# Kernel tuning notes

Measured on AMD Instinct MI355X. Metric: run time of the kernel, lower is better.

The kernel has to match this reference:

```python
import jax, jax.numpy as jnp
import numpy as np

CLIP = 100000.0
T, N, C, H, E = 8, 1024, 64, 256, 32768
NC = N * (N + 1) // 2


def _ntn(t):
    return jnp.nan_to_num(t, nan=0.0, posinf=CLIP, neginf=-CLIP)


def _gcn_conv(x, row, col, ew, W, b, n):
    # PyG GCNConv: sym-normalized aggregation (self-loops already appended)
    h = x @ W  # [n, out]
    deg = jax.ops.segment_sum(ew, col, num_segments=n)
    dinv = jnp.where(deg > 0, jax.lax.rsqrt(jnp.where(deg > 0, deg, 1.0)), 0.0)
    norm = dinv[row] * ew * dinv[col]  # [e]
    out = jax.ops.segment_sum(norm[:, None] * h[row], col, num_segments=n)
    return out + b


def setup_inputs() -> dict:
    key = jax.random.key(0)
    ks = jax.random.split(key, 10)
    return {
        "xs": jax.random.normal(ks[0], (T, N, C), jnp.float32),
        "edge_index": jax.random.randint(ks[1], (T, 2, E), 0, N),
        "edge_weight": jax.random.uniform(ks[2], (T, E), jnp.float32),
        "conv1_w": jax.random.normal(ks[3], (C, H), jnp.float32) * 0.05,
        "conv1_b": jnp.zeros((H,), jnp.float32),
        "conv2_w": jax.random.normal(ks[4], (H, H), jnp.float32) * 0.05,
        "conv2_b": jnp.zeros((H,), jnp.float32),
        "w_ih": jax.random.normal(ks[5], (4 * H, H), jnp.float32) * 0.05,
        "w_hh": jax.random.normal(ks[6], (4 * H, H), jnp.float32) * 0.05,
        "b_ih": jnp.zeros((4 * H,), jnp.float32),
        "b_hh": jnp.zeros((4 * H,), jnp.float32),
        "fc_w": jax.random.normal(ks[7], (H, NC), jnp.float32) * 0.02,
        "fc_b": jnp.zeros((NC,), jnp.float32),
    }


def reference(xs, edge_index, edge_weight, conv1_w, conv1_b, conv2_w, conv2_b,
              w_ih, w_hh, b_ih, b_hh, fc_w, fc_b):
    n = xs.shape[1]
    self_idx = jnp.arange(n)

    def per_step(x, ei, ew):
        # add self-loops with weight 1 (GCNConv default)
        row = jnp.concatenate([ei[0], self_idx])
        col = jnp.concatenate([ei[1], self_idx])
        w = jnp.concatenate([ew, jnp.ones((n,), ew.dtype)])
        h = jax.nn.relu(_ntn(_gcn_conv(x, row, col, w, conv1_w, conv1_b, n)))
        h = jax.nn.relu(_ntn(_gcn_conv(h, row, col, w, conv2_w, conv2_b, n)))
        return _ntn(h.mean(axis=0))  # global mean pool, single graph

    embs = _ntn(jax.vmap(per_step)(xs, edge_index, edge_weight))  # [T, H]

    def lstm_step(carry, x_t):
        h, c = carry
        g = x_t @ w_ih.T + b_ih + h @ w_hh.T + b_hh
        i, f, gg, o = jnp.split(g, 4)
        c = jax.nn.sigmoid(f) * c + jax.nn.sigmoid(i) * jnp.tanh(gg)
        h = jax.nn.sigmoid(o) * jnp.tanh(c)
        return (h, c), h

    hdim = w_hh.shape[1]
    init = (jnp.zeros((hdim,), embs.dtype), jnp.zeros((hdim,), embs.dtype))
    _, hs = jax.lax.scan(lstm_step, init, embs)
    final_h = _ntn(_ntn(hs)[-1])  # [H]

    vec = _ntn(final_h @ fc_w + fc_b)  # [N(N+1)/2]
    tril = jnp.tril_indices(n)  # row-major (i, j<=i) matches torch loop
    L = jnp.zeros((n, n), vec.dtype).at[tril].set(vec)
    return _ntn(L @ L.T)
```

## Files before the change

### kernel.cpp

```cpp
#include <hip/hip_runtime.h>
#include <hip/hip_bf16.h>
#include <math.h>

#define T_ 8
#define N_ 1024
#define C_ 64
#define H_ 256
#define E_ 32768
#define NC_ 524800
#define SLACK 96
#define CLIPV 100000.0f

__device__ __forceinline__ float sigmoidf_(float x) { return 1.0f / (1.0f + __expf(-x)); }

__global__ void scatter_direct_kernel(const int* __restrict__ ei, const float* __restrict__ ew,
                                      float* __restrict__ deg, int* __restrict__ cnt,
                                      int* __restrict__ csr_src, float* __restrict__ csr_ew) {
    int g = blockIdx.x * 256 + threadIdx.x;
    int t = g >> 15, e = g & (E_ - 1);
    int row = ei[t * 2 * E_ + e];
    int col = ei[t * 2 * E_ + E_ + e];
    float w = ew[g];
    int bin = t * N_ + col;
    atomicAdd(&deg[bin], w);
    int pos = atomicAdd(&cnt[bin], 1);
    if (pos < SLACK) {
        csr_src[bin * SLACK + pos] = row;
        csr_ew[bin * SLACK + pos] = w;
    }
}

__global__ __launch_bounds__(256) void sgemm_nn(const float* __restrict__ A,
                                                const float* __restrict__ B,
                                                float* __restrict__ C,
                                                int M, int N, int K) {
    __shared__ float As[16][68];
    __shared__ float Bs[16][68];
    int tid = threadIdx.x;
    int tx = tid & 15, ty = tid >> 4;
    int m0 = blockIdx.y * 64, n0 = blockIdx.x * 64;
    float acc[4][4] = {{0.f}};
    for (int k0 = 0; k0 < K; k0 += 16) {
        int ka = tid & 15, ma = tid >> 4;
#pragma unroll
        for (int mm = 0; mm < 64; mm += 16)
            As[ka][ma + mm] = A[(size_t)(m0 + ma + mm) * K + k0 + ka];
        int nb = tid & 63, kb = tid >> 6;
#pragma unroll
        for (int kk = 0; kk < 16; kk += 4)
            Bs[kb + kk][nb] = B[(size_t)(k0 + kb + kk) * N + n0 + nb];
        __syncthreads();
#pragma unroll
        for (int kk = 0; kk < 16; ++kk) {
            float4 a4 = *(const float4*)&As[kk][ty * 4];
            float4 b4 = *(const float4*)&Bs[kk][tx * 4];
            float a[4] = {a4.x, a4.y, a4.z, a4.w};
            float b[4] = {b4.x, b4.y, b4.z, b4.w};
#pragma unroll
            for (int i = 0; i < 4; ++i)
#pragma unroll
                for (int j = 0; j < 4; ++j) acc[i][j] += a[i] * b[j];
        }
        __syncthreads();
    }
#pragma unroll
    for (int i = 0; i < 4; ++i) {
        float4 o = make_float4(acc[i][0], acc[i][1], acc[i][2], acc[i][3]);
        *(float4*)&C[(size_t)(m0 + ty * 4 + i) * N + n0 + tx * 4] = o;
    }
}

template <bool POOL>
__global__ __launch_bounds__(256) void agg_kernel(const float* __restrict__ hin,
                                                  const float* __restrict__ deg,
                                                  const int* __restrict__ cnt,
                                                  const int* __restrict__ csr_src,
                                                  const float* __restrict__ csr_ew,
                                                  const float* __restrict__ bias,
                                                  float* __restrict__ out) {
    __shared__ int s_src[SLACK];
    __shared__ float s_nrm[SLACK];
    int bx = blockIdx.x;
    int t = bx >> 10, j = bx & 1023;
    int c = threadIdx.x;
    float dj = rsqrtf(deg[bx] + 1.0f);
    int count = min(cnt[bx], SLACK);
    const float* hbase = hin + (size_t)(t * N_) * H_;
    const float* dbase = deg + t * N_;
    float self = hin[(size_t)bx * H_ + c];
    if (c < count) {
        int s = csr_src[bx * SLACK + c];
        s_src[c] = s;
        s_nrm[c] = csr_ew[bx * SLACK + c] * rsqrtf(dbase[s] + 1.0f);
    }
    __syncthreads();
    float a0 = 0.f, a1 = 0.f, a2 = 0.f, a3 = 0.f;
    int u = 0;
    for (; u + 3 < count; u += 4) {
        int s0 = s_src[u], s1 = s_src[u + 1], s2 = s_src[u + 2], s3 = s_src[u + 3];
        float n0 = s_nrm[u], n1 = s_nrm[u + 1], n2 = s_nrm[u + 2], n3 = s_nrm[u + 3];
        a0 += n0 * hbase[(size_t)s0 * H_ + c];
        a1 += n1 * hbase[(size_t)s1 * H_ + c];
        a2 += n2 * hbase[(size_t)s2 * H_ + c];
        a3 += n3 * hbase[(size_t)s3 * H_ + c];
    }
    for (; u < count; ++u) a0 += s_nrm[u] * hbase[(size_t)s_src[u] * H_ + c];
    float accE = (a0 + a1) + (a2 + a3);
    float val = dj * (dj * self + accE) + bias[c];
    val = fminf(fmaxf(val, 0.0f), CLIPV);
    if (POOL)
        atomicAdd(&out[(size_t)(t * 32 + (j & 31)) * H_ + c], val * (1.0f / 1024.0f));
    else
        out[(size_t)bx * H_ + c] = val;
}

__global__ __launch_bounds__(256) void xg_pool_kernel(const float* __restrict__ pool_part,
                                                      const float* __restrict__ w_ih,
                                                      const float* __restrict__ b_ih,
                                                      const float* __restrict__ b_hh,
                                                      float* __restrict__ xg) {
    __shared__ float s_e[H_];
    int b = blockIdx.x;
    int t = b >> 2;
    int tid = threadIdx.x;
    int j = (b & 3) * 256 + tid;
    float a = 0.f;
#pragma unroll
    for (int g2 = 0; g2 < 32; ++g2) a += pool_part[(size_t)(t * 32 + g2) * H_ + tid];
    s_e[tid] = fminf(fmaxf(a, -CLIPV), CLIPV);
    __syncthreads();
    const float4* wr = (const float4*)(w_ih + (size_t)j * H_);
    float acc = b_ih[j] + b_hh[j];
#pragma unroll 4
    for (int k4 = 0; k4 < H_ / 4; ++k4) {
        float4 w = wr[k4];
        acc += w.x * s_e[k4 * 4] + w.y * s_e[k4 * 4 + 1] + w.z * s_e[k4 * 4 + 2] + w.w * s_e[k4 * 4 + 3];
    }
    xg[t * 1024 + j] = acc;
}

__device__ __forceinline__ void gbar(int* bar, int target) {
    __syncthreads();
    if (threadIdx.x == 0) {
        __threadfence();
        __hip_atomic_fetch_add(bar, 1, __ATOMIC_ACQ_REL, __HIP_MEMORY_SCOPE_AGENT);
        long spin = 0;
        while (__hip_atomic_load(bar, __ATOMIC_ACQUIRE, __HIP_MEMORY_SCOPE_AGENT) < target) {
            if (++spin > (1L << 27)) break;
        }
    }
    __syncthreads();
}

__global__ __launch_bounds__(1024) void lstm_all_kernel(const float* __restrict__ xg,
                                                        const float* __restrict__ w_hh,
                                                        float* __restrict__ gbuf,
                                                        int* __restrict__ bar,
                                                        float* __restrict__ final_h) {
    __shared__ float s_h[H_];
    int tid = threadIdx.x;
    int jl = tid >> 2, q = tid & 3;
    int j = blockIdx.x * 256 + jl;
    float4 wreg[16];
    const float4* wr = (const float4*)(w_hh + (size_t)j * H_ + q * 64);
#pragma unroll
    for (int r = 0; r < 16; ++r) wreg[r] = wr[r];
    float c_reg = 0.f;
    for (int s = 0; s < T_; ++s) {
        if (s == 0) {
            if (tid < 256) s_h[tid] = 0.f;
        } else {
            if (tid < 256) {
                const float* gp = gbuf + ((s - 1) & 1) * 1024;
                float gi = gp[tid], gf = gp[256 + tid], gg = gp[512 + tid], go = gp[768 + tid];
                c_reg = sigmoidf_(gf) * c_reg + sigmoidf_(gi) * tanhf(gg);
                s_h[tid] = sigmoidf_(go) * tanhf(c_reg);
            }
        }
        __syncthreads();
        float acc = 0.f;
#pragma unroll
        for (int r = 0; r < 16; ++r) {
            float4 w = wreg[r];
            int k = q * 64 + r * 4;
            acc += w.x * s_h[k] + w.y * s_h[k + 1] + w.z * s_h[k + 2] + w.w * s_h[k + 3];
        }
        acc += __shfl_xor(acc, 1);
        acc += __shfl_xor(acc, 2);
        if (q == 0) gbuf[(s & 1) * 1024 + j] = xg[s * 1024 + j] + acc;
        gbar(bar, 4 * (s + 1));
    }
    if (blockIdx.x == 0 && tid < 256) {
        const float* gp = gbuf + ((T_ - 1) & 1) * 1024;
        float gi = gp[tid], gf = gp[256 + tid], gg = gp[512 + tid], go = gp[768 + tid];
        float cc = sigmoidf_(gf) * c_reg + sigmoidf_(gi) * tanhf(gg);
        final_h[tid] = sigmoidf_(go) * tanhf(cc);
    }
}

__device__ __forceinline__ void store_quad(float4 v, int j0, float* __restrict__ Lm) {
    int i = (int)((sqrtf(8.0f * (float)j0 + 1.0f) - 1.0f) * 0.5f);
    while ((i + 1) * (i + 2) / 2 <= j0) ++i;
    while (i * (i + 1) / 2 > j0) --i;
    int rb = i * (i + 1) / 2, col = j0 - rb;
    if (col + 3 <= i) {
        *(float4*)&Lm[(size_t)i * 1024 + col] = v;
    } else {
        float vv[4] = {v.x, v.y, v.z, v.w};
#pragma unroll
        for (int e = 0; e < 4; ++e) {
            int jj = j0 + e;
            while ((i + 1) * (i + 2) / 2 <= jj) ++i;
            Lm[(size_t)i * 1024 + (jj - i * (i + 1) / 2)] = vv[e];
        }
    }
}

__global__ __launch_bounds__(256) void fc_kernel(const float* __restrict__ final_h,
                                                 const float* __restrict__ fc_w,
                                                 const float* __restrict__ fc_b,
                                                 float* __restrict__ Lm) {
    __shared__ float s_h[H_];
    __shared__ float4 s_red[256];
    int tid = threadIdx.x;
    s_h[tid] = final_h[tid];
    __syncthreads();
    const int NQ = NC_ / 4;
    int lane = tid & 63, grp = tid >> 6;
    int j4 = blockIdx.x * 64 + lane;
    const float4* w4 = (const float4*)fc_w;
    float4 acc = make_float4(0.f, 0.f, 0.f, 0.f);
    int k0 = grp * 64;
#pragma unroll 8
    for (int i = 0; i < 64; ++i) {
        int k = k0 + i;
        float4 w = w4[(size_t)k * NQ + j4];
        float hk = s_h[k];
        acc.x += hk * w.x; acc.y += hk * w.y; acc.z += hk * w.z; acc.w += hk * w.w;
    }
    s_red[tid] = acc;
    __syncthreads();
    if (tid < 64) {
        float4 a0 = s_red[tid], a1 = s_red[64 + tid], a2 = s_red[128 + tid], a3 = s_red[192 + tid];
        float4 b = ((const float4*)fc_b)[j4];
        float4 r;
        r.x = a0.x + a1.x + a2.x + a3.x + b.x;
        r.y = a0.y + a1.y + a2.y + a3.y + b.y;
        r.z = a0.z + a1.z + a2.z + a3.z + b.z;
        r.w = a0.w + a1.w + a2.w + a3.w + b.w;
        r.x = fminf(fmaxf(r.x, -CLIPV), CLIPV);
        r.y = fminf(fmaxf(r.y, -CLIPV), CLIPV);
        r.z = fminf(fmaxf(r.z, -CLIPV), CLIPV);
        r.w = fminf(fmaxf(r.w, -CLIPV), CLIPV);
        store_quad(r, j4 * 4, Lm);
    }
}

__global__ __launch_bounds__(256) void syrk_kernel(const float* __restrict__ L, float* __restrict__ Cout) {
    int b = blockIdx.x;
    int I = (int)((sqrtf(8.0f * b + 1.0f) - 1.0f) * 0.5f);
    while ((I + 1) * (I + 2) / 2 <= b) ++I;
    while (I * (I + 1) / 2 > b) --I;
    int J = b - I * (I + 1) / 2;
    int Klim = (J + 1) * 64;
    int kbeg = blockIdx.y * 256;
    int kend = min(Klim, kbeg + 256);
    if (kbeg >= kend) return;

    __shared__ float As[16][68];
    __shared__ float Bs[16][68];
    int tid = threadIdx.x;
    int tx = tid & 15, ty = tid >> 4;
    int m0 = I * 64, n0 = J * 64;
    float acc[4][4] = {{0.f}};
    for (int k0 = kbeg; k0 < kend; k0 += 16) {
        int ka = tid & 15, ma = tid >> 4;
#pragma unroll
        for (int mm = 0; mm < 64; mm += 16) {
            As[ka][ma + mm] = L[(size_t)(m0 + ma + mm) * 1024 + k0 + ka];
            Bs[ka][ma + mm] = L[(size_t)(n0 + ma + mm) * 1024 + k0 + ka];
        }
        __syncthreads();
#pragma unroll
        for (int kk = 0; kk < 16; ++kk) {
            float4 a4 = *(const float4*)&As[kk][ty * 4];
            float4 b4 = *(const float4*)&Bs[kk][tx * 4];
            float a[4] = {a4.x, a4.y, a4.z, a4.w};
            float bb[4] = {b4.x, b4.y, b4.z, b4.w};
#pragma unroll
            for (int i = 0; i < 4; ++i)
#pragma unroll
                for (int j = 0; j < 4; ++j) acc[i][j] += a[i] * bb[j];
        }
        __syncthreads();
    }
#pragma unroll
    for (int i = 0; i < 4; ++i)
#pragma unroll
        for (int j = 0; j < 4; ++j)
            atomicAdd(&Cout[(size_t)(m0 + ty * 4 + i) * 1024 + n0 + tx * 4 + j], acc[i][j]);
}

__global__ __launch_bounds__(256) void mirror_kernel(float* __restrict__ Cout) {
    int J = blockIdx.x, I = blockIdx.y;
    if (J >= I) return;
    __shared__ float s[64][65];
    int cc = threadIdx.x & 63, r0 = threadIdx.x >> 6;
    for (int r = r0; r < 64; r += 4)
        s[r][cc] = Cout[(size_t)(I * 64 + r) * 1024 + J * 64 + cc];
    __syncthreads();
    for (int r = r0; r < 64; r += 4)
        Cout[(size_t)(J * 64 + r) * 1024 + I * 64 + cc] = s[cc][r];
}

extern "C" void kernel_launch(void* const* d_in, const int* in_sizes, int n_in,
                              void* d_out, int out_size, void* d_ws, size_t ws_size,
                              hipStream_t stream) {
    const float* xs      = (const float*)d_in[0];
    const int*   ei      = (const int*)d_in[1];
    const float* ew      = (const float*)d_in[2];
    const float* conv1_w = (const float*)d_in[3];
    const float* conv1_b = (const float*)d_in[4];
    const float* conv2_w = (const float*)d_in[5];
    const float* conv2_b = (const float*)d_in[6];
    const float* w_ih    = (const float*)d_in[7];
    const float* w_hh    = (const float*)d_in[8];
    const float* b_ih    = (const float*)d_in[9];
    const float* b_hh    = (const float*)d_in[10];
    const float* fc_w    = (const float*)d_in[11];
    const float* fc_b    = (const float*)d_in[12];
    float* out = (float*)d_out;

    float* ws = (float*)d_ws;
    size_t off = 0;
    float* xw1  = ws + off; off += (size_t)T_ * N_ * H_;
    float* h1   = ws + off; off += (size_t)T_ * N_ * H_;
    float* Lm   = ws + off; off += (size_t)N_ * N_;
    float* deg  = ws + off; off += T_ * N_;
    int*   cnt  = (int*)(ws + off); off += T_ * N_;
    float* pool_part = ws + off; off += T_ * 32 * H_;
    int*   bar  = (int*)(ws + off); off += 256;
    size_t zero_bytes = ((size_t)N_ * N_ + (size_t)(T_ * N_) * 2 + T_ * 32 * H_ + 256) * 4;
    float* zero_base = Lm;
    float* csr_ew = ws + off; off += (size_t)T_ * N_ * SLACK;
    float* xg   = ws + off; off += T_ * 4 * H_;
    float* gbuf = ws + off; off += 2 * 1024;
    float* final_h = ws + off; off += 256;
    int* csr_src = (int*)(ws + off); off += (size_t)T_ * N_ * SLACK;
    (void)ws_size; (void)in_sizes; (void)n_in; (void)out_size;

    hipMemsetAsync(zero_base, 0, zero_bytes, stream);
    hipMemsetAsync(out, 0, (size_t)N_ * N_ * sizeof(float), stream);

    scatter_direct_kernel<<<(T_ * E_) / 256, 256, 0, stream>>>(ei, ew, deg, cnt, csr_src, csr_ew);

    sgemm_nn<<<dim3(H_ / 64, (T_ * N_) / 64), 256, 0, stream>>>(xs, conv1_w, xw1, T_ * N_, H_, C_);
    agg_kernel<false><<<T_ * N_, 256, 0, stream>>>(xw1, deg, cnt, csr_src, csr_ew, conv1_b, h1);
    sgemm_nn<<<dim3(H_ / 64, (T_ * N_) / 64), 256, 0, stream>>>(h1, conv2_w, xw1, T_ * N_, H_, H_);
    agg_kernel<true><<<T_ * N_, 256, 0, stream>>>(xw1, deg, cnt, csr_src, csr_ew, conv2_b, pool_part);

    xg_pool_kernel<<<32, 256, 0, stream>>>(pool_part, w_ih, b_ih, b_hh, xg);
    lstm_all_kernel<<<4, 1024, 0, stream>>>(xg, w_hh, gbuf, bar, final_h);

    fc_kernel<<<NC_ / 4 / 64, 256, 0, stream>>>(final_h, fc_w, fc_b, Lm);

    syrk_kernel<<<dim3(136, 4), 256, 0, stream>>>(Lm, out);
    mirror_kernel<<<dim3(16, 16), 256, 0, stream>>>(out);
}
```

Before: 307.8 us.

## Pack CSR, vectorize aggregation, fuse input projection into LSTM, skip Lm memset

Edge source and weight are packed into one int2 CSR array. The aggregation kernel now handles four nodes per block with float4 loads per lane. The pooling-sum and W_ih projection kernel is folded into the persistent LSTM kernel, which removes one launch and the xg round trip. The 4 MB Lm memset is replaced by masking the upper triangle inside syrk, and a small zero-init kernel clears only deg, cnt, pool and the barrier. This trades extra compare/select in syrk and more redundant pool reads across the LSTM blocks for less memset traffic and fewer launches.

```diff
diff --git a/kernel.cpp b/kernel.cpp
--- a/kernel.cpp
+++ b/kernel.cpp
@@ -13,9 +13,14 @@
 
 __device__ __forceinline__ float sigmoidf_(float x) { return 1.0f / (1.0f + __expf(-x)); }
 
+__global__ void zero_init_kernel(float* base, int n) {
+    int g = blockIdx.x * 256 + threadIdx.x;
+    if (g < n) base[g] = 0.0f;
+}
+
 __global__ void scatter_direct_kernel(const int* __restrict__ ei, const float* __restrict__ ew,
                                       float* __restrict__ deg, int* __restrict__ cnt,
-                                      int* __restrict__ csr_src, float* __restrict__ csr_ew) {
+                                      int2* __restrict__ csr) {
     int g = blockIdx.x * 256 + threadIdx.x;
     int t = g >> 15, e = g & (E_ - 1);
     int row = ei[t * 2 * E_ + e];
@@ -25,8 +30,8 @@
     atomicAdd(&deg[bin], w);
     int pos = atomicAdd(&cnt[bin], 1);
     if (pos < SLACK) {
-        csr_src[bin * SLACK + pos] = row;
-        csr_ew[bin * SLACK + pos] = w;
+        int2 v; v.x = row; v.y = __float_as_int(w);
+        csr[bin * SLACK + pos] = v;
     }
 }
 
@@ -74,69 +79,65 @@
 __global__ __launch_bounds__(256) void agg_kernel(const float* __restrict__ hin,
                                                   const float* __restrict__ deg,
                                                   const int* __restrict__ cnt,
-                                                  const int* __restrict__ csr_src,
-                                                  const float* __restrict__ csr_ew,
+                                                  const int2* __restrict__ csr,
                                                   const float* __restrict__ bias,
                                                   float* __restrict__ out) {
-    __shared__ int s_src[SLACK];
-    __shared__ float s_nrm[SLACK];
-    int bx = blockIdx.x;
+    __shared__ int s_src[4][SLACK];
+    __shared__ float s_nrm[4][SLACK];
+    int tid = threadIdx.x;
+    int nd = tid >> 6, lane = tid & 63;
+    int bx = blockIdx.x * 4 + nd;
     int t = bx >> 10, j = bx & 1023;
-    int c = threadIdx.x;
+    int lane4 = lane * 4;
     float dj = rsqrtf(deg[bx] + 1.0f);
     int count = min(cnt[bx], SLACK);
     const float* hbase = hin + (size_t)(t * N_) * H_;
     const float* dbase = deg + t * N_;
-    float self = hin[(size_t)bx * H_ + c];
-    if (c < count) {
-        int s = csr_src[bx * SLACK + c];
-        s_src[c] = s;
-        s_nrm[c] = csr_ew[bx * SLACK + c] * rsqrtf(dbase[s] + 1.0f);
-    }
-    __syncthreads();
-    float a0 = 0.f, a1 = 0.f, a2 = 0.f, a3 = 0.f;
+    float4 self = *(const float4*)&hin[(size_t)bx * H_ + lane4];
+    for (int u = lane; u < count; u += 64) {
+        int2 v = csr[bx * SLACK + u];
+        s_src[nd][u] = v.x;
+        s_nrm[nd][u] = __int_as_float(v.y) * rsqrtf(dbase[v.x] + 1.0f);
+    }
+    __syncthreads();
+    float4 a0 = {0,0,0,0}, a1 = {0,0,0,0}, a2 = {0,0,0,0}, a3 = {0,0,0,0};
     int u = 0;
     for (; u + 3 < count; u += 4) {
-        int s0 = s_src[u], s1 = s_src[u + 1], s2 = s_src[u + 2], s3 = s_src[u + 3];
-        float n0 = s_nrm[u], n1 = s_nrm[u + 1], n2 = s_nrm[u + 2], n3 = s_nrm[u + 3];
-        a0 += n0 * hbase[(size_t)s0 * H_ + c];
-        a1 += n1 * hbase[(size_t)s1 * H_ + c];
-        a2 += n2 * hbase[(size_t)s2 * H_ + c];
-        a3 += n3 * hbase[(size_t)s3 * H_ + c];
-    }
-    for (; u < count; ++u) a0 += s_nrm[u] * hbase[(size_t)s_src[u] * H_ + c];
-    float accE = (a0 + a1) + (a2 + a3);
-    float val = dj * (dj * self + accE) + bias[c];
-    val = fminf(fmaxf(val, 0.0f), CLIPV);
-    if (POOL)
-        atomicAdd(&out[(size_t)(t * 32 + (j & 31)) * H_ + c], val * (1.0f / 1024.0f));
-    else
-        out[(size_t)bx * H_ + c] = val;
-}
-
-__global__ __launch_bounds__(256) void xg_pool_kernel(const float* __restrict__ pool_part,
-                                                      const float* __restrict__ w_ih,
-                                                      const float* __restrict__ b_ih,
-                                                      const float* __restrict__ b_hh,
-                                                      float* __restrict__ xg) {
-    __shared__ float s_e[H_];
-    int b = blockIdx.x;
-    int t = b >> 2;
-    int tid = threadIdx.x;
-    int j = (b & 3) * 256 + tid;
-    float a = 0.f;
-#pragma unroll
-    for (int g2 = 0; g2 < 32; ++g2) a += pool_part[(size_t)(t * 32 + g2) * H_ + tid];
-    s_e[tid] = fminf(fmaxf(a, -CLIPV), CLIPV);
-    __syncthreads();
-    const float4* wr = (const float4*)(w_ih + (size_t)j * H_);
-    float acc = b_ih[j] + b_hh[j];
-#pragma unroll 4
-    for (int k4 = 0; k4 < H_ / 4; ++k4) {
-        float4 w = wr[k4];
-        acc += w.x * s_e[k4 * 4] + w.y * s_e[k4 * 4 + 1] + w.z * s_e[k4 * 4 + 2] + w.w * s_e[k4 * 4 + 3];
-    }
-    xg[t * 1024 + j] = acc;
+        int s0 = s_src[nd][u], s1 = s_src[nd][u+1], s2 = s_src[nd][u+2], s3 = s_src[nd][u+3];
+        float n0 = s_nrm[nd][u], n1 = s_nrm[nd][u+1], n2 = s_nrm[nd][u+2], n3 = s_nrm[nd][u+3];
+        float4 v0 = *(const float4*)&hbase[(size_t)s0 * H_ + lane4];
+        float4 v1 = *(const float4*)&hbase[(size_t)s1 * H_ + lane4];
+        float4 v2 = *(const float4*)&hbase[(size_t)s2 * H_ + lane4];
+        float4 v3 = *(const float4*)&hbase[(size_t)s3 * H_ + lane4];
+        a0.x += n0*v0.x; a0.y += n0*v0.y; a0.z += n0*v0.z; a0.w += n0*v0.w;
+        a1.x += n1*v1.x; a1.y += n1*v1.y; a1.z += n1*v1.z; a1.w += n1*v1.w;
+        a2.x += n2*v2.x; a2.y += n2*v2.y; a2.z += n2*v2.z; a2.w += n2*v2.w;
+        a3.x += n3*v3.x; a3.y += n3*v3.y; a3.z += n3*v3.z; a3.w += n3*v3.w;
+    }
+    for (; u < count; ++u) {
+        int s0 = s_src[nd][u]; float n0 = s_nrm[nd][u];
+        float4 v0 = *(const float4*)&hbase[(size_t)s0 * H_ + lane4];
+        a0.x += n0*v0.x; a0.y += n0*v0.y; a0.z += n0*v0.z; a0.w += n0*v0.w;
+    }
+    float4 bi = *(const float4*)&bias[lane4];
+    float4 val;
+    val.x = dj * (dj * self.x + ((a0.x + a1.x) + (a2.x + a3.x))) + bi.x;
+    val.y = dj * (dj * self.y + ((a0.y + a1.y) + (a2.y + a3.y))) + bi.y;
+    val.z = dj * (dj * self.z + ((a0.z + a1.z) + (a2.z + a3.z))) + bi.z;
+    val.w = dj * (dj * self.w + ((a0.w + a1.w) + (a2.w + a3.w))) + bi.w;
+    val.x = fminf(fmaxf(val.x, 0.0f), CLIPV);
+    val.y = fminf(fmaxf(val.y, 0.0f), CLIPV);
+    val.z = fminf(fmaxf(val.z, 0.0f), CLIPV);
+    val.w = fminf(fmaxf(val.w, 0.0f), CLIPV);
+    if (POOL) {
+        float* p = &out[(size_t)(t * 32 + (j & 31)) * H_ + lane4];
+        atomicAdd(p + 0, val.x * (1.0f / 1024.0f));
+        atomicAdd(p + 1, val.y * (1.0f / 1024.0f));
+        atomicAdd(p + 2, val.z * (1.0f / 1024.0f));
+        atomicAdd(p + 3, val.w * (1.0f / 1024.0f));
+    } else {
+        *(float4*)&out[(size_t)bx * H_ + lane4] = val;
+    }
 }
 
 __device__ __forceinline__ void gbar(int* bar, int target) {
@@ -152,19 +153,58 @@
     __syncthreads();
 }
 
-__global__ __launch_bounds__(1024) void lstm_all_kernel(const float* __restrict__ xg,
-                                                        const float* __restrict__ w_hh,
-                                                        float* __restrict__ gbuf,
-                                                        int* __restrict__ bar,
-                                                        float* __restrict__ final_h) {
+__global__ __launch_bounds__(1024) void lstm_fused_kernel(const float* __restrict__ pool_part,
+                                                          const float* __restrict__ w_ih,
+                                                          const float* __restrict__ w_hh,
+                                                          const float* __restrict__ b_ih,
+                                                          const float* __restrict__ b_hh,
+                                                          float* __restrict__ gbuf,
+                                                          int* __restrict__ bar,
+                                                          float* __restrict__ final_h) {
+    __shared__ float s_emb[T_][H_];
+    __shared__ float s_xg[T_][256];
     __shared__ float s_h[H_];
     int tid = threadIdx.x;
     int jl = tid >> 2, q = tid & 3;
     int j = blockIdx.x * 256 + jl;
-    float4 wreg[16];
-    const float4* wr = (const float4*)(w_hh + (size_t)j * H_ + q * 64);
-#pragma unroll
-    for (int r = 0; r < 16; ++r) wreg[r] = wr[r];
+    for (int v = tid; v < T_ * H_; v += 1024) {
+        int t = v >> 8, ch = v & 255;
+        float a = 0.f;
+#pragma unroll
+        for (int g2 = 0; g2 < 32; ++g2) a += pool_part[(size_t)(t * 32 + g2) * H_ + ch];
+        s_emb[t][ch] = fminf(fmaxf(a, -CLIPV), CLIPV);
+    }
+    __syncthreads();
+    {
+        const float4* wr = (const float4*)(w_ih + (size_t)j * H_ + q * 64);
+        float acc_t[T_] = {0.f, 0.f, 0.f, 0.f, 0.f, 0.f, 0.f, 0.f};
+#pragma unroll
+        for (int r = 0; r < 16; ++r) {
+            float4 w = wr[r];
+            int k = q * 64 + r * 4;
+#pragma unroll
+            for (int t = 0; t < T_; ++t)
+                acc_t[t] += w.x * s_emb[t][k] + w.y * s_emb[t][k + 1]
+                          + w.z * s_emb[t][k + 2] + w.w * s_emb[t][k + 3];
+        }
+#pragma unroll
+        for (int t = 0; t < T_; ++t) {
+            acc_t[t] += __shfl_xor(acc_t[t], 1);
+            acc_t[t] += __shfl_xor(acc_t[t], 2);
+        }
+        if (q == 0) {
+            float bias = b_ih[j] + b_hh[j];
+#pragma unroll
+            for (int t = 0; t < T_; ++t) s_xg[t][jl] = bias + acc_t[t];
+        }
+    }
+    float4 whh[16];
+    {
+        const float4* wr = (const float4*)(w_hh + (size_t)j * H_ + q * 64);
+#pragma unroll
+        for (int r = 0; r < 16; ++r) whh[r] = wr[r];
+    }
+    __syncthreads();
     float c_reg = 0.f;
     for (int s = 0; s < T_; ++s) {
         if (s == 0) {
@@ -181,13 +221,13 @@
         float acc = 0.f;
 #pragma unroll
         for (int r = 0; r < 16; ++r) {
-            float4 w = wreg[r];
+            float4 w = whh[r];
             int k = q * 64 + r * 4;
             acc += w.x * s_h[k] + w.y * s_h[k + 1] + w.z * s_h[k + 2] + w.w * s_h[k + 3];
         }
         acc += __shfl_xor(acc, 1);
         acc += __shfl_xor(acc, 2);
-        if (q == 0) gbuf[(s & 1) * 1024 + j] = xg[s * 1024 + j] + acc;
+        if (q == 0) gbuf[(s & 1) * 1024 + j] = s_xg[s][jl] + acc;
         gbar(bar, 4 * (s + 1));
     }
     if (blockIdx.x == 0 && tid < 256) {
@@ -277,8 +317,11 @@
         int ka = tid & 15, ma = tid >> 4;
 #pragma unroll
         for (int mm = 0; mm < 64; mm += 16) {
-            As[ka][ma + mm] = L[(size_t)(m0 + ma + mm) * 1024 + k0 + ka];
-            Bs[ka][ma + mm] = L[(size_t)(n0 + ma + mm) * 1024 + k0 + ka];
+            int rA = m0 + ma + mm, rB = n0 + ma + mm, kg = k0 + ka;
+            float va = L[(size_t)rA * 1024 + kg];
+            float vb = L[(size_t)rB * 1024 + kg];
+            As[ka][ma + mm] = (kg <= rA) ? va : 0.f;
+            Bs[ka][ma + mm] = (kg <= rB) ? vb : 0.f;
         }
         __syncthreads();
 #pragma unroll
@@ -340,30 +383,26 @@
     int*   cnt  = (int*)(ws + off); off += T_ * N_;
     float* pool_part = ws + off; off += T_ * 32 * H_;
     int*   bar  = (int*)(ws + off); off += 256;
-    size_t zero_bytes = ((size_t)N_ * N_ + (size_t)(T_ * N_) * 2 + T_ * 32 * H_ + 256) * 4;
-    float* zero_base = Lm;
-    float* csr_ew = ws + off; off += (size_t)T_ * N_ * SLACK;
-    float* xg   = ws + off; off += T_ * 4 * H_;
+    int zero_elems = T_ * N_ * 2 + T_ * 32 * H_ + 256;
+    float* zero_base = deg;
     float* gbuf = ws + off; off += 2 * 1024;
     float* final_h = ws + off; off += 256;
-    int* csr_src = (int*)(ws + off); off += (size_t)T_ * N_ * SLACK;
+    int2* csr = (int2*)(ws + off); off += (size_t)T_ * N_ * SLACK * 2;
     (void)ws_size; (void)in_sizes; (void)n_in; (void)out_size;
 
-    hipMemsetAsync(zero_base, 0, zero_bytes, stream);
+    zero_init_kernel<<<(zero_elems + 255) / 256, 256, 0, stream>>>(zero_base, zero_elems);
+    scatter_direct_kernel<<<(T_ * E_) / 256, 256, 0, stream>>>(ei, ew, deg, cnt, csr);
+
+    sgemm_nn<<<dim3(H_ / 64, (T_ * N_) / 64), 256, 0, stream>>>(xs, conv1_w, xw1, T_ * N_, H_, C_);
+    agg_kernel<false><<<T_ * N_ / 4, 256, 0, stream>>>(xw1, deg, cnt, csr, conv1_b, h1);
+    sgemm_nn<<<dim3(H_ / 64, (T_ * N_) / 64), 256, 0, stream>>>(h1, conv2_w, xw1, T_ * N_, H_, H_);
+    agg_kernel<true><<<T_ * N_ / 4, 256, 0, stream>>>(xw1, deg, cnt, csr, conv2_b, pool_part);
+
+    lstm_fused_kernel<<<4, 1024, 0, stream>>>(pool_part, w_ih, w_hh, b_ih, b_hh, gbuf, bar, final_h);
+
+    fc_kernel<<<NC_ / 4 / 64, 256, 0, stream>>>(final_h, fc_w, fc_b, Lm);
+
     hipMemsetAsync(out, 0, (size_t)N_ * N_ * sizeof(float), stream);
-
-    scatter_direct_kernel<<<(T_ * E_) / 256, 256, 0, stream>>>(ei, ew, deg, cnt, csr_src, csr_ew);
-
-    sgemm_nn<<<dim3(H_ / 64, (T_ * N_) / 64), 256, 0, stream>>>(xs, conv1_w, xw1, T_ * N_, H_, C_);
-    agg_kernel<false><<<T_ * N_, 256, 0, stream>>>(xw1, deg, cnt, csr_src, csr_ew, conv1_b, h1);
-    sgemm_nn<<<dim3(H_ / 64, (T_ * N_) / 64), 256, 0, stream>>>(h1, conv2_w, xw1, T_ * N_, H_, H_);
-    agg_kernel<true><<<T_ * N_, 256, 0, stream>>>(xw1, deg, cnt, csr_src, csr_ew, conv2_b, pool_part);
-
-    xg_pool_kernel<<<32, 256, 0, stream>>>(pool_part, w_ih, b_ih, b_hh, xg);
-    lstm_all_kernel<<<4, 1024, 0, stream>>>(xg, w_hh, gbuf, bar, final_h);
-
-    fc_kernel<<<NC_ / 4 / 64, 256, 0, stream>>>(final_h, fc_w, fc_b, Lm);
-
     syrk_kernel<<<dim3(136, 4), 256, 0, stream>>>(Lm, out);
     mirror_kernel<<<dim3(16, 16), 256, 0, stream>>>(out);
 }
```

Measured after the change: 325.5 us. 5.8% more time.
